# Kernel tuning notes

Hardware: AMD Instinct MI355X
Metric: run time of the kernel (lower is better)

Reference implementation:

```python
import jax, jax.numpy as jnp
import numpy as np

N = 100000   # nodes
E = 300000   # directed edges
NG = 4096    # graphs in batch
F_IN = 22
HID = 128


def setup_inputs() -> dict:
    key = jax.random.key(0)
    ks = jax.random.split(key, 32)
    s = 0.05
    inp = {
        "x": jax.random.normal(ks[0], (N, F_IN), jnp.float32),
        "edge_index": jax.random.randint(ks[1], (2, E), 0, N),
        "batch": jnp.sort(jax.random.randint(ks[2], (N,), 0, NG)),
        # GAT layer 1: 22 -> 4 heads x 32
        "W1": jax.random.normal(ks[3], (F_IN, HID), jnp.float32) * s,
        "as1": jax.random.normal(ks[4], (4, 32), jnp.float32) * s,
        "ad1": jax.random.normal(ks[5], (4, 32), jnp.float32) * s,
        "b1": jnp.zeros((HID,), jnp.float32),
        "g1": jnp.ones((HID,), jnp.float32),
        "be1": jnp.zeros((HID,), jnp.float32),
        # GAT layer 2: 128 -> 4 heads x 32
        "W2": jax.random.normal(ks[6], (HID, HID), jnp.float32) * s,
        "as2": jax.random.normal(ks[7], (4, 32), jnp.float32) * s,
        "ad2": jax.random.normal(ks[8], (4, 32), jnp.float32) * s,
        "b2": jnp.zeros((HID,), jnp.float32),
        "g2": jnp.ones((HID,), jnp.float32),
        "be2": jnp.zeros((HID,), jnp.float32),
        # GAT layer 3: 128 -> 1 head x 128
        "W3": jax.random.normal(ks[9], (HID, HID), jnp.float32) * s,
        "as3": jax.random.normal(ks[10], (1, HID), jnp.float32) * s,
        "ad3": jax.random.normal(ks[11], (1, HID), jnp.float32) * s,
        "b3": jnp.zeros((HID,), jnp.float32),
        "g3": jnp.ones((HID,), jnp.float32),
        "be3": jnp.zeros((HID,), jnp.float32),
        # MLP head
        "fw1": jax.random.normal(ks[12], (HID, 64), jnp.float32) * s,
        "fb1": jnp.zeros((64,), jnp.float32),
        "fw2": jax.random.normal(ks[13], (64, 1), jnp.float32) * s,
        "fb2": jnp.zeros((1,), jnp.float32),
    }
    return inp


def reference(x, edge_index, batch, W1, as1, ad1, b1, g1, be1,
              W2, as2, ad2, b2, g2, be2, W3, as3, ad3, b3, g3, be3,
              fw1, fb1, fw2, fb2):
    n = x.shape[0]
    sl = jnp.arange(n)
    src = jnp.concatenate([edge_index[0], sl])  # PyG GATConv adds self-loops
    dst = jnp.concatenate([edge_index[1], sl])

    def gat(h_in, W, a_s, a_d, b):
        H, C = a_s.shape
        h = (h_in @ W).reshape(n, H, C)                      # [N,H,C]
        al_s = jnp.einsum('nhc,hc->nh', h, a_s)              # per-node src score
        al_d = jnp.einsum('nhc,hc->nh', h, a_d)
        e = jax.nn.leaky_relu(al_s[src] + al_d[dst], 0.2)    # [Etot,H]
        emax = jax.ops.segment_max(e, dst, num_segments=n)
        ex = jnp.exp(e - emax[dst])
        den = jax.ops.segment_sum(ex, dst, num_segments=n)
        alpha = ex / (den[dst] + 1e-16)                       # segment softmax over in-edges
        msg = h[src] * alpha[:, :, None]                      # [Etot,H,C]
        out = jax.ops.segment_sum(msg, dst, num_segments=n)
        return out.reshape(n, H * C) + b

    def bn(h, g, be):
        m = h.mean(0)
        v = h.var(0)
        return (h - m) * jax.lax.rsqrt(v + 1e-5) * g + be

    h = jax.nn.relu(bn(gat(x, W1, as1, ad1, b1), g1, be1))
    h = jax.nn.relu(bn(gat(h, W2, as2, ad2, b2), g2, be2))
    h = jax.nn.relu(bn(gat(h, W3, as3, ad3, b3), g3, be3))

    # global mean pool over graphs
    s = jax.ops.segment_sum(h, batch, num_segments=NG)
    cnt = jax.ops.segment_sum(jnp.ones((n,), h.dtype), batch, num_segments=NG)
    pooled = s / jnp.maximum(cnt, 1.0)[:, None]

    z = jax.nn.relu(pooled @ fw1 + fb1)
    return z @ fw2 + fb2
```

## Files before the change

### kernel.cpp

```cpp
#include <hip/hip_runtime.h>

#define N_NODES 100000
#define N_EDGES 300000
#define N_ETOT  400000
#define NGRAPH  4096
#define HID     128
#define NBLK_SCAN 391
#define PNPB    32
#define STATS_BLOCKS 512
#define NSLICE  64

typedef __attribute__((ext_vector_type(8))) short short8;
typedef __attribute__((ext_vector_type(8))) ushort ushort8;
typedef __attribute__((ext_vector_type(4))) float f32x4;

__device__ __forceinline__ ushort f2bf(float f) {
    union { float f; unsigned u; } x; x.f = f;
    unsigned r = x.u + 0x7FFF + ((x.u >> 16) & 1);
    return (ushort)(r >> 16);
}

__device__ __forceinline__ float bf2f(ushort v) {
    union { unsigned u; float f; } t;
    t.u = ((unsigned)v) << 16;
    return t.f;
}

__device__ __forceinline__ float2 bf2f2(unsigned v) {
    union { unsigned u; float f; } lo, hi;
    lo.u = v << 16;
    hi.u = v & 0xFFFF0000u;
    return make_float2(lo.f, hi.f);
}

__global__ __launch_bounds__(256) void setup_kernel(
    const float* __restrict__ x,
    const float* __restrict__ W1, const float* __restrict__ W2, const float* __restrict__ W3,
    ushort* __restrict__ Wt1, ushort* __restrict__ Wt2, ushort* __restrict__ Wt3,
    ushort* __restrict__ Xb, float* __restrict__ sums_sl, int* __restrict__ counts,
    float* __restrict__ pooled)
{
    const int i = blockIdx.x * 256 + threadIdx.x;
    if (i < 16384) {
        int c = i >> 7, k = i & 127;
        Wt2[c * 128 + k] = f2bf(W2[k * 128 + c]);
    } else if (i < 32768) {
        int j = i - 16384; int c = j >> 7, k = j & 127;
        Wt3[c * 128 + k] = f2bf(W3[k * 128 + c]);
    } else if (i < 36864) {
        int j = i - 32768; int c = j >> 5, k = j & 31;
        Wt1[c * 32 + k] = (k < 22) ? f2bf(W1[k * 128 + c]) : (ushort)0;
    } else if (i < 36864 + N_NODES * 32) {
        int j = i - 36864; int n = j >> 5, k = j & 31;
        Xb[j] = (k < 22) ? f2bf(x[n * 22 + k]) : (ushort)0;
    } else if (i < 36864 + N_NODES * 32 + NSLICE * 256) {
        sums_sl[i - (36864 + N_NODES * 32)] = 0.f;
    } else if (i < 36864 + N_NODES * 32 + NSLICE * 256 + N_NODES) {
        counts[i - (36864 + N_NODES * 32 + NSLICE * 256)] = 0;
    } else if (i < 36864 + N_NODES * 32 + NSLICE * 256 + N_NODES + NGRAPH * HID + NGRAPH) {
        pooled[i - (36864 + N_NODES * 32 + NSLICE * 256 + N_NODES)] = 0.f;
    }
}
#define SETUP_TOT (36864 + N_NODES * 32 + NSLICE * 256 + N_NODES + NGRAPH * HID + NGRAPH)

template<int K, bool PRE_BN, int HH>
__global__ __launch_bounds__(256) void mfma_gemm_kernel(
    const ushort* __restrict__ Ab, const ushort* __restrict__ Wt,
    const float* __restrict__ scale, const float* __restrict__ shift,
    const float* __restrict__ avs, const float* __restrict__ avd,
    ushort* __restrict__ Cb, float* __restrict__ als, float* __restrict__ ald, int M)
{
    constexpr int SEGS = K / 8;
    constexpr int SSH  = (K == 128) ? 4 : 2;
    constexpr int SWM  = SEGS - 1;
    constexpr int NP   = SEGS / 2;
    constexpr int KT   = K / 32;

    __shared__ ushort Asm[128 * K];
    __shared__ ushort Bsm[128 * K];

    const int tid  = threadIdx.x;
    const int wave = tid >> 6;
    const int lane = tid & 63;
    const int ln   = lane & 15;
    const int quad = lane >> 4;
    const int wr0  = (wave >> 1) * 64;
    const int wc0  = (wave & 1) * 64;
    const int row0 = blockIdx.x * 128;

    short8 aR[NP], wR[NP];
    #pragma unroll
    for (int q = 0; q < NP; ++q) {
        const int chunk = tid + q * 256;
        const int r   = chunk >> SSH;
        const int seg = chunk & SWM;
        aR[q] = *(const short8*)&Ab[(size_t)(row0 + r) * K + seg * 8];
        wR[q] = *(const short8*)&Wt[(size_t)r * K + seg * 8];
    }
    if constexpr (PRE_BN) {
        #pragma unroll
        for (int q = 0; q < NP; ++q) {
            const int seg = (tid + q * 256) & SWM;
            const int cc  = seg * 8;
            #pragma unroll
            for (int i = 0; i < 8; ++i) {
                float f = bf2f((ushort)aR[q][i]);
                f = fmaxf(f * scale[cc + i] + shift[cc + i], 0.f);
                aR[q][i] = (short)f2bf(f);
            }
        }
    }
    #pragma unroll
    for (int q = 0; q < NP; ++q) {
        const int chunk = tid + q * 256;
        const int r   = chunk >> SSH;
        const int seg = chunk & SWM;
        const int sp  = seg ^ (r & SWM);
        *(short8*)&Asm[r * K + sp * 8] = aR[q];
        *(short8*)&Bsm[r * K + sp * 8] = wR[q];
    }
    __syncthreads();

    f32x4 acc[4][4] = {};
    #pragma unroll
    for (int kt = 0; kt < KT; ++kt) {
        short8 af[4], bf[4];
        #pragma unroll
        for (int i = 0; i < 4; ++i) {
            const int ra = wr0 + i * 16 + ln;
            const int ca = wc0 + i * 16 + ln;
            af[i] = *(const short8*)&Asm[ra * K + (((kt * 4 + quad) ^ (ra & SWM)) * 8)];
            bf[i] = *(const short8*)&Bsm[ca * K + (((kt * 4 + quad) ^ (ca & SWM)) * 8)];
        }
        #pragma unroll
        for (int tr = 0; tr < 4; ++tr)
            #pragma unroll
            for (int tc = 0; tc < 4; ++tc)
                acc[tr][tc] = __builtin_amdgcn_mfma_f32_16x16x32_bf16(
                    af[tr], bf[tc], acc[tr][tc], 0, 0, 0);
    }

    #pragma unroll
    for (int tr = 0; tr < 4; ++tr)
        #pragma unroll
        for (int rg = 0; rg < 4; ++rg) {
            const int gr = row0 + wr0 + tr * 16 + quad * 4 + rg;
            if (gr < M) {
                #pragma unroll
                for (int tc = 0; tc < 4; ++tc)
                    Cb[(size_t)gr * HID + wc0 + tc * 16 + ln] = f2bf(acc[tr][tc][rg]);
            }
        }

    __syncthreads();
    float* ps = (float*)Asm;
    float* pd = (float*)Bsm;
    #pragma unroll
    for (int tr = 0; tr < 4; ++tr)
      #pragma unroll
      for (int rg = 0; rg < 4; ++rg) {
        float sA = 0.f, sB = 0.f, dA = 0.f, dB = 0.f;
        #pragma unroll
        for (int tc = 0; tc < 4; ++tc) {
            const int col = wc0 + tc * 16 + ln;
            const float v = acc[tr][tc][rg];
            if (tc < 2) { sA += v * avs[col]; dA += v * avd[col]; }
            else        { sB += v * avs[col]; dB += v * avd[col]; }
        }
        #pragma unroll
        for (int m = 1; m < 16; m <<= 1) {
            sA += __shfl_xor(sA, m); sB += __shfl_xor(sB, m);
            dA += __shfl_xor(dA, m); dB += __shfl_xor(dB, m);
        }
        if (ln == 0) {
            const int rl = wr0 + tr * 16 + quad * 4 + rg;
            const int h0 = (wave & 1) * 2;
            ps[rl * 4 + h0] = sA; ps[rl * 4 + h0 + 1] = sB;
            pd[rl * 4 + h0] = dA; pd[rl * 4 + h0 + 1] = dB;
        }
      }
    __syncthreads();
    {
        const int r  = tid & 127;
        const int gr = row0 + r;
        if (gr < M) {
            if (tid < 128) {
                if (HH == 4) {
                    #pragma unroll
                    for (int h = 0; h < 4; ++h) als[gr * 4 + h] = ps[r * 4 + h];
                } else als[gr] = ps[r * 4] + ps[r * 4 + 1] + ps[r * 4 + 2] + ps[r * 4 + 3];
            } else {
                if (HH == 4) {
                    #pragma unroll
                    for (int h = 0; h < 4; ++h) ald[gr * 4 + h] = pd[r * 4 + h];
                } else ald[gr] = pd[r * 4] + pd[r * 4 + 1] + pd[r * 4 + 2] + pd[r * 4 + 3];
            }
        }
    }
}

__global__ void hist_kernel(const int* __restrict__ ei, int* __restrict__ counts) {
    int e = blockIdx.x * blockDim.x + threadIdx.x;
    if (e >= N_ETOT) return;
    int dst = (e < N_EDGES) ? ei[N_EDGES + e] : e - N_EDGES;
    atomicAdd(&counts[dst], 1);
}

__global__ __launch_bounds__(256) void scanA_kernel(
    const int* __restrict__ counts, int* __restrict__ rowptr, int* __restrict__ bsum)
{
    __shared__ int ls[256];
    const int t = threadIdx.x;
    const int i = blockIdx.x * 256 + t;
    const int v = (i < N_NODES) ? counts[i] : 0;
    ls[t] = v; __syncthreads();
    #pragma unroll
    for (int off = 1; off < 256; off <<= 1) {
        int add = (t >= off) ? ls[t - off] : 0;
        __syncthreads();
        ls[t] += add;
        __syncthreads();
    }
    if (i < N_NODES) rowptr[i] = ls[t] - v;
    if (t == 255) bsum[blockIdx.x] = ls[255];
}

__global__ __launch_bounds__(512) void scanB_kernel(int* __restrict__ bsum)
{
    __shared__ int ls[512];
    const int t = threadIdx.x;
    const int v = (t < NBLK_SCAN) ? bsum[t] : 0;
    ls[t] = v; __syncthreads();
    #pragma unroll
    for (int off = 1; off < 512; off <<= 1) {
        int add = (t >= off) ? ls[t - off] : 0;
        __syncthreads();
        ls[t] += add;
        __syncthreads();
    }
    if (t < NBLK_SCAN) bsum[t] = ls[t] - v;
}

__global__ void scanC_kernel(int* __restrict__ rowptr, const int* __restrict__ bsum,
                             int* __restrict__ cursor)
{
    int i = blockIdx.x * 256 + threadIdx.x;
    if (i < N_NODES) {
        int v = rowptr[i] + bsum[blockIdx.x];
        rowptr[i] = v;
        cursor[i] = v;
    }
    if (i == 0) rowptr[N_NODES] = N_ETOT;
}

__global__ void scatter_kernel(const int* __restrict__ ei, int* __restrict__ cursor,
                               int* __restrict__ psrc)
{
    int e = blockIdx.x * blockDim.x + threadIdx.x;
    if (e >= N_ETOT) return;
    int src, dst;
    if (e < N_EDGES) { src = ei[e]; dst = ei[N_EDGES + e]; }
    else             { src = dst = e - N_EDGES; }
    int pos = atomicAdd(&cursor[dst], 1);
    psrc[pos] = src;
}

template<int HH>
__global__ __launch_bounds__(256) void agg_kernel(
    const ushort* __restrict__ H, const float* __restrict__ als,
    const float* __restrict__ ald, const int* __restrict__ rowptr,
    const int* __restrict__ psrc, ushort* __restrict__ Outb)
{
    const int tid  = threadIdx.x;
    const int node = blockIdx.x * 4 + (tid >> 6);
    const int lane = tid & 63;
    const int grp  = lane >> 4;
    const int cl   = lane & 15;
    const int hd   = (HH == 4) ? (cl >> 2) : 0;
    const int r0 = rowptr[node];
    const int r1 = rowptr[node + 1];
    const float aldh = (HH == 4) ? ald[node * 4 + hd] : ald[node];

    float den = 0.f;
    float acc[8] = {};
    for (int p = r0 + grp; p < r1; p += 4) {
        const int src = psrc[p];
        float v = ((HH == 4) ? als[src * 4 + hd] : als[src]) + aldh;
        v = (v > 0.f) ? v : 0.2f * v;
        const float ex = __expf(v);
        const uint4 hv = *(const uint4*)&H[(size_t)src * HID + cl * 8];
        const float2 h0 = bf2f2(hv.x), h1 = bf2f2(hv.y);
        const float2 h2 = bf2f2(hv.z), h3 = bf2f2(hv.w);
        acc[0] += ex * h0.x; acc[1] += ex * h0.y;
        acc[2] += ex * h1.x; acc[3] += ex * h1.y;
        acc[4] += ex * h2.x; acc[5] += ex * h2.y;
        acc[6] += ex * h3.x; acc[7] += ex * h3.y;
        den += ex;
    }
    #pragma unroll
    for (int m = 16; m < 64; m <<= 1) {
        den += __shfl_xor(den, m);
        #pragma unroll
        for (int i = 0; i < 8; ++i) acc[i] += __shfl_xor(acc[i], m);
    }
    if (grp == 0) {
        const float inv = 1.f / (den + 1e-16f);
        ushort8 o;
        #pragma unroll
        for (int i = 0; i < 8; ++i) o[i] = f2bf(acc[i] * inv);
        *(ushort8*)&Outb[(size_t)node * HID + cl * 8] = o;
    }
}

__global__ __launch_bounds__(256) void bn_stats_kernel(
    const ushort* __restrict__ X, float* __restrict__ sums_sl)
{
    __shared__ float ls[16][128], lq[16][128];
    const int tid = threadIdx.x;
    const int ro  = tid >> 4;
    const int ci  = tid & 15;
    const int c0  = ci * 8;
    const int rpb = (N_NODES + STATS_BLOCKS - 1) / STATS_BLOCKS;
    const int r0  = blockIdx.x * rpb;
    const int r1  = min(r0 + rpb, N_NODES);

    float s[8] = {}, q[8] = {};
    for (int r = r0 + ro; r < r1; r += 16) {
        const ushort8 v = *(const ushort8*)&X[(size_t)r * HID + c0];
        #pragma unroll
        for (int j = 0; j < 8; ++j) {
            const float f = bf2f(v[j]);
            s[j] += f; q[j] += f * f;
        }
    }
    #pragma unroll
    for (int j = 0; j < 8; ++j) { ls[ro][c0 + j] = s[j]; lq[ro][c0 + j] = q[j]; }
    __syncthreads();
    const int half = tid >> 7;
    const int c    = tid & 127;
    float acc = 0.f;
    if (half == 0) {
        #pragma unroll
        for (int k = 0; k < 16; ++k) acc += ls[k][c];
    } else {
        #pragma unroll
        for (int k = 0; k < 16; ++k) acc += lq[k][c];
    }
    atomicAdd(&sums_sl[(blockIdx.x & (NSLICE - 1)) * 256 + tid], acc);
}

__global__ __launch_bounds__(256) void bn_finalize_kernel(
    float* __restrict__ sums_sl,
    const float* __restrict__ g, const float* __restrict__ be,
    float* __restrict__ scale, float* __restrict__ shift)
{
    __shared__ float red[256];
    const int tid = threadIdx.x;
    float s = 0.f;
    for (int b = 0; b < NSLICE; ++b) {
        s += sums_sl[b * 256 + tid];
        sums_sl[b * 256 + tid] = 0.f;
    }
    red[tid] = s;
    __syncthreads();
    if (tid < 128) {
        const float m = red[tid] * (1.f / N_NODES);
        const float v = red[tid + 128] * (1.f / N_NODES) - m * m;
        const float sc = g[tid] * rsqrtf(v + 1e-5f);
        scale[tid] = sc;
        shift[tid] = be[tid] - m * sc;
    }
}

__global__ __launch_bounds__(128) void bn_pool_kernel(
    const ushort* __restrict__ X, const float* __restrict__ scale, const float* __restrict__ shift,
    const int* __restrict__ batch, float* __restrict__ pooled, float* __restrict__ cnt)
{
    const int c = threadIdx.x;
    const int n0 = blockIdx.x * PNPB;
    const int n1 = min(n0 + PNPB, N_NODES);
    const float sc = scale[c], sh = shift[c];
    int gcur = batch[n0];
    float acc = 0.f;
    int run = 0;
    for (int n = n0; n < n1; ++n) {
        const int g = batch[n];
        if (g != gcur) {
            atomicAdd(&pooled[(size_t)gcur * HID + c], acc);
            if (c == 0) atomicAdd(&cnt[gcur], (float)run);
            acc = 0.f; run = 0; gcur = g;
        }
        const float v = bf2f(X[(size_t)n * HID + c]) * sc + sh;
        acc += fmaxf(v, 0.f);
        ++run;
    }
    atomicAdd(&pooled[(size_t)gcur * HID + c], acc);
    if (c == 0) atomicAdd(&cnt[gcur], (float)run);
}

__global__ __launch_bounds__(256) void mlp_kernel(
    const float* __restrict__ pooled, const float* __restrict__ cnt,
    const float* __restrict__ fw1, const float* __restrict__ fb1,
    const float* __restrict__ fw2, const float* __restrict__ fb2,
    float* __restrict__ out)
{
    __shared__ float w1[HID * 64];
    __shared__ float rows[4][HID];
    const int tid = threadIdx.x;
    for (int i = tid; i < HID * 64; i += 256) w1[i] = fw1[i];
    const int gl = tid >> 6;
    const int j  = tid & 63;
    const float b1 = fb1[j];
    const float w2 = fw2[j];
    __syncthreads();
    #pragma unroll
    for (int it = 0; it < 4; ++it) {
        const int g = blockIdx.x * 16 + it * 4 + gl;
        const float inv = 1.f / fmaxf(cnt[g], 1.f);
        rows[gl][j]      = pooled[(size_t)g * HID + j] * inv;
        rows[gl][j + 64] = pooled[(size_t)g * HID + 64 + j] * inv;
        __syncthreads();
        float z = b1;
        #pragma unroll 8
        for (int c2 = 0; c2 < HID; ++c2) z += rows[gl][c2] * w1[c2 * 64 + j];
        z = fmaxf(z, 0.f);
        float p = z * w2;
        #pragma unroll
        for (int off = 32; off; off >>= 1) p += __shfl_down(p, off);
        if (j == 0) out[g] = p + fb2[0];
        __syncthreads();
    }
}

extern "C" void kernel_launch(void* const* d_in, const int* in_sizes, int n_in,
                              void* d_out, int out_size, void* d_ws, size_t ws_size,
                              hipStream_t stream)
{
    const float* x     = (const float*)d_in[0];
    const int*   ei    = (const int*)d_in[1];
    const int*   batch = (const int*)d_in[2];
    const float* W1  = (const float*)d_in[3];
    const float* as1 = (const float*)d_in[4];
    const float* ad1 = (const float*)d_in[5];
    const float* g1  = (const float*)d_in[7];
    const float* be1 = (const float*)d_in[8];
    const float* W2  = (const float*)d_in[9];
    const float* as2 = (const float*)d_in[10];
    const float* ad2 = (const float*)d_in[11];
    const float* g2  = (const float*)d_in[13];
    const float* be2 = (const float*)d_in[14];
    const float* W3  = (const float*)d_in[15];
    const float* as3 = (const float*)d_in[16];
    const float* ad3 = (const float*)d_in[17];
    const float* g3  = (const float*)d_in[19];
    const float* be3 = (const float*)d_in[20];
    const float* fw1 = (const float*)d_in[21];
    const float* fb1 = (const float*)d_in[22];
    const float* fw2 = (const float*)d_in[23];
    const float* fb2 = (const float*)d_in[24];
    float* out = (float*)d_out;

    ushort* Hb  = (ushort*)d_ws;
    ushort* Bh  = Hb  + (size_t)N_NODES * HID;
    ushort* Xb  = Bh  + (size_t)N_NODES * HID;
    ushort* Wt1 = Xb  + (size_t)N_NODES * 32;
    ushort* Wt2 = Wt1 + 128 * 32;
    ushort* Wt3 = Wt2 + 128 * 128;
    float* als    = (float*)(Wt3 + 128 * 128);
    float* ald    = als + (size_t)N_NODES * 4;
    float* sums_sl= ald + (size_t)N_NODES * 4;
    float* scale  = sums_sl + NSLICE * 256;
    float* shift  = scale + HID;
    float* pooled = shift + HID;
    float* cnt    = pooled + (size_t)NGRAPH * HID;
    int*   rowptr = (int*)(cnt + NGRAPH);
    int*   counts = rowptr + (N_NODES + 1);
    int*   cursor = counts + N_NODES;
    int*   bsum   = cursor + N_NODES;
    int*   psrc   = bsum + 512;

    auto cdiv = [](int a, int b) { return (a + b - 1) / b; };

    setup_kernel<<<cdiv(SETUP_TOT, 256), 256, 0, stream>>>(
        x, W1, W2, W3, Wt1, Wt2, Wt3, Xb, sums_sl, counts, pooled);

    hist_kernel<<<cdiv(N_ETOT, 256), 256, 0, stream>>>(ei, counts);
    scanA_kernel<<<NBLK_SCAN, 256, 0, stream>>>(counts, rowptr, bsum);
    scanB_kernel<<<1, 512, 0, stream>>>(bsum);
    scanC_kernel<<<NBLK_SCAN, 256, 0, stream>>>(rowptr, bsum, cursor);
    scatter_kernel<<<cdiv(N_ETOT, 256), 256, 0, stream>>>(ei, cursor, psrc);

    const int ggrid = cdiv(N_NODES, 128);
    const int agrid = N_NODES / 4;

    mfma_gemm_kernel<32, false, 4><<<ggrid, 256, 0, stream>>>(
        Xb, Wt1, nullptr, nullptr, as1, ad1, Hb, als, ald, N_NODES);
    agg_kernel<4><<<agrid, 256, 0, stream>>>(Hb, als, ald, rowptr, psrc, Bh);
    bn_stats_kernel<<<STATS_BLOCKS, 256, 0, stream>>>(Bh, sums_sl);
    bn_finalize_kernel<<<1, 256, 0, stream>>>(sums_sl, g1, be1, scale, shift);

    mfma_gemm_kernel<128, true, 4><<<ggrid, 256, 0, stream>>>(
        Bh, Wt2, scale, shift, as2, ad2, Hb, als, ald, N_NODES);
    agg_kernel<4><<<agrid, 256, 0, stream>>>(Hb, als, ald, rowptr, psrc, Bh);
    bn_stats_kernel<<<STATS_BLOCKS, 256, 0, stream>>>(Bh, sums_sl);
    bn_finalize_kernel<<<1, 256, 0, stream>>>(sums_sl, g2, be2, scale, shift);

    mfma_gemm_kernel<128, true, 1><<<ggrid, 256, 0, stream>>>(
        Bh, Wt3, scale, shift, as3, ad3, Hb, als, ald, N_NODES);
    agg_kernel<1><<<agrid, 256, 0, stream>>>(Hb, als, ald, rowptr, psrc, Bh);
    bn_stats_kernel<<<STATS_BLOCKS, 256, 0, stream>>>(Bh, sums_sl);
    bn_finalize_kernel<<<1, 256, 0, stream>>>(sums_sl, g3, be3, scale, shift);

    bn_pool_kernel<<<cdiv(N_NODES, PNPB), 128, 0, stream>>>(Bh, scale, shift, batch, pooled, cnt);
    mlp_kernel<<<NGRAPH / 16, 256, 0, stream>>>(pooled, cnt, fw1, fb1, fw2, fb2, out);
}
```

Before: 366.4 us.

## Merge edge histogram into first GEMM launch and fold BN finalize via ticket

Two launch-fusion changes. The edge-degree histogram now runs as extra blocks of the first-layer GEMM kernel. The separate single-block BN finalize kernel is folded into bn_stats through a last-block-done ticket counter, which also zeroes the partial sums for the next layer. Together these remove four kernel launches and their serialization gaps, at the cost of an extra atomic ticket, a threadfence per block, and tail work done by the last-arriving block.

```diff
diff --git a/kernel.cpp b/kernel.cpp
--- a/kernel.cpp
+++ b/kernel.cpp
@@ -38,7 +38,7 @@
     const float* __restrict__ W1, const float* __restrict__ W2, const float* __restrict__ W3,
     ushort* __restrict__ Wt1, ushort* __restrict__ Wt2, ushort* __restrict__ Wt3,
     ushort* __restrict__ Xb, float* __restrict__ sums_sl, int* __restrict__ counts,
-    float* __restrict__ pooled)
+    float* __restrict__ pooled, int* __restrict__ ticket)
 {
     const int i = blockIdx.x * 256 + threadIdx.x;
     if (i < 16384) {
@@ -59,16 +59,19 @@
         counts[i - (36864 + N_NODES * 32 + NSLICE * 256)] = 0;
     } else if (i < 36864 + N_NODES * 32 + NSLICE * 256 + N_NODES + NGRAPH * HID + NGRAPH) {
         pooled[i - (36864 + N_NODES * 32 + NSLICE * 256 + N_NODES)] = 0.f;
-    }
-}
-#define SETUP_TOT (36864 + N_NODES * 32 + NSLICE * 256 + N_NODES + NGRAPH * HID + NGRAPH)
+    } else if (i == 36864 + N_NODES * 32 + NSLICE * 256 + N_NODES + NGRAPH * HID + NGRAPH) {
+        *ticket = 0;
+    }
+}
+#define SETUP_TOT (36864 + N_NODES * 32 + NSLICE * 256 + N_NODES + NGRAPH * HID + NGRAPH + 1)
 
 template<int K, bool PRE_BN, int HH>
-__global__ __launch_bounds__(256) void mfma_gemm_kernel(
+__device__ __forceinline__ void gemm_body(
     const ushort* __restrict__ Ab, const ushort* __restrict__ Wt,
     const float* __restrict__ scale, const float* __restrict__ shift,
     const float* __restrict__ avs, const float* __restrict__ avd,
-    ushort* __restrict__ Cb, float* __restrict__ als, float* __restrict__ ald, int M)
+    ushort* __restrict__ Cb, float* __restrict__ als, float* __restrict__ ald,
+    int M, int blk)
 {
     constexpr int SEGS = K / 8;
     constexpr int SSH  = (K == 128) ? 4 : 2;
@@ -86,7 +89,7 @@
     const int quad = lane >> 4;
     const int wr0  = (wave >> 1) * 64;
     const int wc0  = (wave & 1) * 64;
-    const int row0 = blockIdx.x * 128;
+    const int row0 = blk * 128;
 
     short8 aR[NP], wR[NP];
     #pragma unroll
@@ -199,11 +202,31 @@
     }
 }
 
-__global__ void hist_kernel(const int* __restrict__ ei, int* __restrict__ counts) {
-    int e = blockIdx.x * blockDim.x + threadIdx.x;
-    if (e >= N_ETOT) return;
-    int dst = (e < N_EDGES) ? ei[N_EDGES + e] : e - N_EDGES;
-    atomicAdd(&counts[dst], 1);
+template<int K, bool PRE_BN, int HH>
+__global__ __launch_bounds__(256) void mfma_gemm_kernel(
+    const ushort* __restrict__ Ab, const ushort* __restrict__ Wt,
+    const float* __restrict__ scale, const float* __restrict__ shift,
+    const float* __restrict__ avs, const float* __restrict__ avd,
+    ushort* __restrict__ Cb, float* __restrict__ als, float* __restrict__ ald, int M)
+{
+    gemm_body<K, PRE_BN, HH>(Ab, Wt, scale, shift, avs, avd, Cb, als, ald, M, blockIdx.x);
+}
+
+__global__ __launch_bounds__(256) void gemm1_hist_kernel(
+    const ushort* __restrict__ Ab, const ushort* __restrict__ Wt,
+    const float* __restrict__ avs, const float* __restrict__ avd,
+    ushort* __restrict__ Cb, float* __restrict__ als, float* __restrict__ ald,
+    int M, int gemmBlocks, const int* __restrict__ ei, int* __restrict__ counts)
+{
+    if ((int)blockIdx.x >= gemmBlocks) {
+        const int e = (blockIdx.x - gemmBlocks) * 256 + threadIdx.x;
+        if (e < N_ETOT) {
+            const int dst = (e < N_EDGES) ? ei[N_EDGES + e] : e - N_EDGES;
+            atomicAdd(&counts[dst], 1);
+        }
+        return;
+    }
+    gemm_body<32, false, 4>(Ab, Wt, nullptr, nullptr, avs, avd, Cb, als, ald, M, blockIdx.x);
 }
 
 __global__ __launch_bounds__(256) void scanA_kernel(
@@ -313,9 +336,13 @@
 }
 
 __global__ __launch_bounds__(256) void bn_stats_kernel(
-    const ushort* __restrict__ X, float* __restrict__ sums_sl)
+    const ushort* __restrict__ X, float* __restrict__ sums_sl,
+    const float* __restrict__ g, const float* __restrict__ be,
+    float* __restrict__ scale, float* __restrict__ shift, int* __restrict__ ticket)
 {
     __shared__ float ls[16][128], lq[16][128];
+    __shared__ float red[256];
+    __shared__ int lastFlag;
     const int tid = threadIdx.x;
     const int ro  = tid >> 4;
     const int ci  = tid & 15;
@@ -347,28 +374,28 @@
         for (int k = 0; k < 16; ++k) acc += lq[k][c];
     }
     atomicAdd(&sums_sl[(blockIdx.x & (NSLICE - 1)) * 256 + tid], acc);
-}
-
-__global__ __launch_bounds__(256) void bn_finalize_kernel(
-    float* __restrict__ sums_sl,
-    const float* __restrict__ g, const float* __restrict__ be,
-    float* __restrict__ scale, float* __restrict__ shift)
-{
-    __shared__ float red[256];
-    const int tid = threadIdx.x;
-    float s = 0.f;
-    for (int b = 0; b < NSLICE; ++b) {
-        s += sums_sl[b * 256 + tid];
-        sums_sl[b * 256 + tid] = 0.f;
-    }
-    red[tid] = s;
-    __syncthreads();
-    if (tid < 128) {
-        const float m = red[tid] * (1.f / N_NODES);
-        const float v = red[tid + 128] * (1.f / N_NODES) - m * m;
-        const float sc = g[tid] * rsqrtf(v + 1e-5f);
-        scale[tid] = sc;
-        shift[tid] = be[tid] - m * sc;
+    __threadfence();
+    __syncthreads();
+    if (tid == 0) lastFlag = (atomicAdd(ticket, 1) == STATS_BLOCKS - 1);
+    __syncthreads();
+    if (lastFlag) {
+        float t = 0.f;
+        for (int b = 0; b < NSLICE; ++b) {
+            t += __hip_atomic_load(&sums_sl[b * 256 + tid], __ATOMIC_RELAXED,
+                                   __HIP_MEMORY_SCOPE_AGENT);
+            __hip_atomic_store(&sums_sl[b * 256 + tid], 0.f, __ATOMIC_RELAXED,
+                               __HIP_MEMORY_SCOPE_AGENT);
+        }
+        red[tid] = t;
+        __syncthreads();
+        if (tid < 128) {
+            const float m = red[tid] * (1.f / N_NODES);
+            const float v = red[tid + 128] * (1.f / N_NODES) - m * m;
+            const float sc = g[tid] * rsqrtf(v + 1e-5f);
+            scale[tid] = sc;
+            shift[tid] = be[tid] - m * sc;
+        }
+        if (tid == 0) *ticket = 0;
     }
 }
 
@@ -477,39 +504,38 @@
     int*   counts = rowptr + (N_NODES + 1);
     int*   cursor = counts + N_NODES;
     int*   bsum   = cursor + N_NODES;
-    int*   psrc   = bsum + 512;
+    int*   ticket = bsum + 512;
+    int*   psrc   = ticket + 1;
 
     auto cdiv = [](int a, int b) { return (a + b - 1) / b; };
 
     setup_kernel<<<cdiv(SETUP_TOT, 256), 256, 0, stream>>>(
-        x, W1, W2, W3, Wt1, Wt2, Wt3, Xb, sums_sl, counts, pooled);
-
-    hist_kernel<<<cdiv(N_ETOT, 256), 256, 0, stream>>>(ei, counts);
+        x, W1, W2, W3, Wt1, Wt2, Wt3, Xb, sums_sl, counts, pooled, ticket);
+
+    const int ggrid = cdiv(N_NODES, 128);
+    const int hgrid = cdiv(N_ETOT, 256);
+    const int agrid = N_NODES / 4;
+
+    gemm1_hist_kernel<<<ggrid + hgrid, 256, 0, stream>>>(
+        Xb, Wt1, as1, ad1, Hb, als, ald, N_NODES, ggrid, ei, counts);
+
     scanA_kernel<<<NBLK_SCAN, 256, 0, stream>>>(counts, rowptr, bsum);
     scanB_kernel<<<1, 512, 0, stream>>>(bsum);
     scanC_kernel<<<NBLK_SCAN, 256, 0, stream>>>(rowptr, bsum, cursor);
     scatter_kernel<<<cdiv(N_ETOT, 256), 256, 0, stream>>>(ei, cursor, psrc);
 
-    const int ggrid = cdiv(N_NODES, 128);
-    const int agrid = N_NODES / 4;
-
-    mfma_gemm_kernel<32, false, 4><<<ggrid, 256, 0, stream>>>(
-        Xb, Wt1, nullptr, nullptr, as1, ad1, Hb, als, ald, N_NODES);
     agg_kernel<4><<<agrid, 256, 0, stream>>>(Hb, als, ald, rowptr, psrc, Bh);
-    bn_stats_kernel<<<STATS_BLOCKS, 256, 0, stream>>>(Bh, sums_sl);
-    bn_finalize_kernel<<<1, 256, 0, stream>>>(sums_sl, g1, be1, scale, shift);
+    bn_stats_kernel<<<STATS_BLOCKS, 256, 0, stream>>>(Bh, sums_sl, g1, be1, scale, shift, ticket);
 
     mfma_gemm_kernel<128, true, 4><<<ggrid, 256, 0, stream>>>(
         Bh, Wt2, scale, shift, as2, ad2, Hb, als, ald, N_NODES);
     agg_kernel<4><<<agrid, 256, 0, stream>>>(Hb, als, ald, rowptr, psrc, Bh);
-    bn_stats_kernel<<<STATS_BLOCKS, 256, 0, stream>>>(Bh, sums_sl);
-    bn_finalize_kernel<<<1, 256, 0, stream>>>(sums_sl, g2, be2, scale, shift);
+    bn_stats_kernel<<<STATS_BLOCKS, 256, 0, stream>>>(Bh, sums_sl, g2, be2, scale, shift, ticket);
 
     mfma_gemm_kernel<128, true, 1><<<ggrid, 256, 0, stream>>>(
         Bh, Wt3, scale, shift, as3, ad3, Hb, als, ald, N_NODES);
     agg_kernel<1><<<agrid, 256, 0, stream>>>(Hb, als, ald, rowptr, psrc, Bh);
-    bn_stats_kernel<<<STATS_BLOCKS, 256, 0, stream>>>(Bh, sums_sl);
-    bn_finalize_kernel<<<1, 256, 0, stream>>>(sums_sl, g3, be3, scale, shift);
+    bn_stats_kernel<<<STATS_BLOCKS, 256, 0, stream>>>(Bh, sums_sl, g3, be3, scale, shift, ticket);
 
     bn_pool_kernel<<<cdiv(N_NODES, PNPB), 128, 0, stream>>>(Bh, scale, shift, batch, pooled, cnt);
     mlp_kernel<<<NGRAPH / 16, 256, 0, stream>>>(pooled, cnt, fw1, fb1, fw2, fb2, out);
```

Result: slower. 492.5 us (+34.4%).
